# Optimization experiments

Hardware: AMD Instinct MI355X
Metric: run time of the kernel (lower is better)

Reference implementation:

```python
import jax, jax.numpy as jnp
import numpy as np

LATENT = 128
HEADS = 4
HEAD_DIM = LATENT // HEADS
NUM_BUCKETS = 32
MAX_DISTANCE = 100000
B, N = 8, 2048


def relative_position_bucket(qpos, kpos):
    """T5-style bidirectional relative position bucketing.
    qpos, kpos: [B, N] int -> buckets [B, N, N] int32 in [0, NUM_BUCKETS).
    """
    rel = kpos[:, None, :] - qpos[:, :, None]  # [B, Nq, Nk]
    half = NUM_BUCKETS // 2
    buckets = (rel > 0).astype(jnp.int32) * half
    arel = jnp.abs(rel)
    max_exact = half // 2
    is_small = arel < max_exact
    # log-spaced buckets for larger distances
    large = max_exact + (
        jnp.log(jnp.maximum(arel, 1).astype(jnp.float32) / max_exact)
        / np.log(MAX_DISTANCE / max_exact)
        * (half - max_exact)
    ).astype(jnp.int32)
    large = jnp.minimum(large, half - 1)
    return buckets + jnp.where(is_small, arel.astype(jnp.int32), large)


def setup_inputs() -> dict:
    key = jax.random.key(0)
    ks = jax.random.split(key, 12)
    s = 0.02
    x = jax.random.normal(ks[0], (B, N, LATENT), dtype=jnp.float32)
    positions = jnp.sort(jax.random.randint(ks[1], (B, N), 0, 1000000), axis=-1)
    mask = jnp.ones((B, N), dtype=bool)
    Wq = jax.random.normal(ks[2], (LATENT, LATENT), dtype=jnp.float32) * s
    bq = jax.random.normal(ks[3], (LATENT,), dtype=jnp.float32) * s
    Wk = jax.random.normal(ks[4], (LATENT, LATENT), dtype=jnp.float32) * s
    bk = jax.random.normal(ks[5], (LATENT,), dtype=jnp.float32) * s
    Wv = jax.random.normal(ks[6], (LATENT, LATENT), dtype=jnp.float32) * s
    bv = jax.random.normal(ks[7], (LATENT,), dtype=jnp.float32) * s
    pos_w = jax.random.normal(ks[8], (NUM_BUCKETS + 1, HEADS), dtype=jnp.float32) * s
    Wo = jax.random.normal(ks[9], (LATENT, LATENT), dtype=jnp.float32) * s
    bo = jax.random.normal(ks[10], (LATENT,), dtype=jnp.float32) * s
    return {"x": x, "positions": positions, "mask": mask,
            "Wq": Wq, "bq": bq, "Wk": Wk, "bk": bk, "Wv": Wv, "bv": bv,
            "pos_w": pos_w, "Wo": Wo, "bo": bo}


def reference(x, positions, mask, Wq, bq, Wk, bk, Wv, bv, pos_w, Wo, bo):
    b, n, _ = x.shape
    # QKV projections, split heads: [b, h, n, d]
    Q = (x @ Wq + bq).reshape(b, n, HEADS, HEAD_DIM).transpose(0, 2, 1, 3)
    K = (x @ Wk + bk).reshape(b, n, HEADS, HEAD_DIM).transpose(0, 2, 1, 3)
    V = (x @ Wv + bv).reshape(b, n, HEADS, HEAD_DIM).transpose(0, 2, 1, 3)
    scores = jnp.einsum("bhqd,bhkd->bhqk", Q, K) / jnp.sqrt(
        jnp.asarray(HEAD_DIM, dtype=x.dtype))
    buckets = relative_position_bucket(positions, positions)  # [b, n, n]
    bias = pos_w[buckets]                  # [b, n, n, h]
    scores = scores + bias.transpose(0, 3, 1, 2)  # [b, h, n, n]
    scores = jnp.where(mask[:, None, None, :], scores, -jnp.inf)
    attn = jax.nn.softmax(scores, axis=-1)
    attn = jnp.nan_to_num(attn, nan=0.0)
    attended = jnp.einsum("bhqk,bhkd->bhqd", attn, V)
    attended = attended.transpose(0, 2, 1, 3).reshape(b, n, LATENT)
    return attended @ Wo + bo
```

## Files before the change

### kernel.cpp

```cpp
#include <hip/hip_runtime.h>
#include <math.h>


#define LOG2E 1.4426950408889634f
#define QKV_SCALE 0.17677669529663687f
#define QS (QKV_SCALE * LOG2E)

typedef _Float16 half8 __attribute__((ext_vector_type(8)));
typedef float ffrag __attribute__((ext_vector_type(4)));

#if __has_builtin(__builtin_amdgcn_exp2f)
#define EXP2F __builtin_amdgcn_exp2f
#else
#define EXP2F exp2f
#endif

static __device__ __forceinline__ unsigned short f16bits(float f) {
    return __builtin_bit_cast(unsigned short, (_Float16)f);
}
static __device__ __forceinline__ float h16f(unsigned int bits) {
    return (float)__builtin_bit_cast(_Float16, (unsigned short)(bits & 0xFFFFu));
}
static __device__ __forceinline__ unsigned int pk2(float a, float b) {
    return __builtin_bit_cast(unsigned int, __builtin_amdgcn_cvt_pkrtz(a, b));
}
static __device__ __forceinline__ void async_cp16(const unsigned short* g, unsigned short* l) {
    __builtin_amdgcn_global_load_lds(
        (const __attribute__((address_space(1))) unsigned int*)g,
        (__attribute__((address_space(3))) unsigned int*)l, 16, 0, 0);
}

__device__ __constant__ int SN_TAB[32] = {
     -2000000000,
    -30755, -9458, -2908, -894, -275, -84, -26,
    -7, -6, -5, -4, -3, -2, -1,
    0,
    1, 2, 3, 4, 5, 6, 7,
    8,
    27, 85, 276, 895, 2909, 9459, 30756,
    2000000000 };

__global__ __launch_bounds__(256)
void prep_seg_kernel(const float* __restrict__ Wq, const float* __restrict__ Wk,
                     const float* __restrict__ Wv, const float* __restrict__ Wo,
                     const float* __restrict__ bq, const float* __restrict__ bk,
                     const float* __restrict__ bv,
                     const int* __restrict__ positions,
                     unsigned short* __restrict__ Wt_qkv,
                     unsigned short* __restrict__ Wt_o,
                     float* __restrict__ bias_qkv,
                     unsigned int* __restrict__ segtab)
{
    if (blockIdx.x < 256) {
        const int e = blockIdx.x * 256 + threadIdx.x;
        const int m = e >> 14, r = e & 16383;
        const int c = r >> 7, k = r & 127;
        float v;
        if (m == 0)      v = Wq[k * 128 + c] * QS;
        else if (m == 1) v = Wk[k * 128 + c];
        else if (m == 2) v = Wv[k * 128 + c];
        else             v = Wo[k * 128 + c];
        if (m < 3) Wt_qkv[(m * 128 + c) * 128 + k] = f16bits(v);
        else       Wt_o[c * 128 + k] = f16bits(v);
        if (e < 128)      bias_qkv[e] = bq[e] * QS;
        else if (e < 256) bias_qkv[e] = bk[e - 128];
        else if (e < 384) bias_qkv[e] = bv[e - 256];
        return;
    }
    const int gid = (blockIdx.x - 256) * 256 + threadIdx.x;
    const int row = gid >> 5;
    const int s = gid & 31;
    const int b = row >> 11;
    const int* kp = positions + b * 2048;
    const int qp = kp[row & 2047];
    const int bucket = (s < 15) ? (15 - s) : (s == 15 ? 0 : s + 1);
    if (s == 31) { segtab[row * 32 + s] = (2048u << 16) | 31u; return; }
    const int target = qp + SN_TAB[s + 1];
    int lo = 0, hi = 2048;
    while (lo < hi) { const int mid = (lo + hi) >> 1; if (kp[mid] < target) lo = mid + 1; else hi = mid; }
    segtab[row * 32 + s] = ((unsigned)lo << 16) | (unsigned)bucket;
}

__global__ __launch_bounds__(512)
void qkv_mfma(const float* __restrict__ x, const unsigned short* __restrict__ Wt,
              const float* __restrict__ bias_qkv,
              unsigned short* __restrict__ Qb, unsigned short* __restrict__ Kb,
              unsigned short* __restrict__ Vg2)
{
    __shared__ __align__(16) unsigned short Xs[64 * 136];
    const int tid = threadIdx.x;
    const int token0 = blockIdx.x * 64;
    #pragma unroll
    for (int it = 0; it < 4; ++it) {
        const int f = tid + it * 512;
        const int row = f >> 5, k0 = (f & 31) << 2;
        const float4 xv = *(const float4*)(x + (size_t)(token0 + row) * 128 + k0);
        uint2 u;
        u.x = pk2(xv.x, xv.y);
        u.y = pk2(xv.z, xv.w);
        *(uint2*)(Xs + row * 136 + k0) = u;
    }
    __syncthreads();

    const int wave = tid >> 6, lane = tid & 63;
    const int lq = lane & 15, quad = lane >> 4;
    const int b = token0 >> 11;
    const int n0 = token0 & 2047;

    #pragma unroll
    for (int j = 0; j < 3; ++j) {
        const int ct = wave + j * 8;
        const int colbase = ct * 16;
        half8 wf[4];
        #pragma unroll
        for (int ks = 0; ks < 4; ++ks)
            wf[ks] = *(const half8*)(Wt + (colbase + lq) * 128 + ks * 32 + quad * 8);

        if (ct < 16) {
            const int c0q = colbase + quad * 4;
            const float4 bv = *(const float4*)(bias_qkv + c0q);
            #pragma unroll
            for (int msub = 0; msub < 4; ++msub) {
                ffrag acc = {bv.x, bv.y, bv.z, bv.w};
                #pragma unroll
                for (int ks = 0; ks < 4; ++ks) {
                    const half8 xf = *(const half8*)(Xs + (msub * 16 + lq) * 136 + ks * 32 + quad * 8);
                    acc = __builtin_amdgcn_mfma_f32_16x16x32_f16(wf[ks], xf, acc, 0, 0, 0);
                }
                const int n = n0 + msub * 16 + lq;
                const int c0 = c0q & 127;
                const int h = c0 >> 5, d = c0 & 31;
                const ushort4 v4 = make_ushort4(f16bits(acc[0]), f16bits(acc[1]),
                                                f16bits(acc[2]), f16bits(acc[3]));
                unsigned short* base = (ct < 8) ? Qb : Kb;
                *(ushort4*)(base + ((size_t)(b * 4 + h) * 2048 + n) * 32 + d) = v4;
            }
        } else {
            const float bias = bias_qkv[colbase + lq];
            const int c2 = colbase + lq - 256;
            const int h = c2 >> 5, d = c2 & 31;
            const size_t bhh = (size_t)(b * 4 + h);
            #pragma unroll
            for (int msub = 0; msub < 4; ++msub) {
                ffrag acc = {bias, bias, bias, bias};
                #pragma unroll
                for (int ks = 0; ks < 4; ++ks) {
                    const half8 xf = *(const half8*)(Xs + (msub * 16 + lq) * 136 + ks * 32 + quad * 8);
                    acc = __builtin_amdgcn_mfma_f32_16x16x32_f16(xf, wf[ks], acc, 0, 0, 0);
                }
                const int n = n0 + msub * 16 + quad * 4;
                const int chunk = n >> 7, kloc = n & 127;
                const int win = kloc >> 5, rem = kloc & 31;
                const int half = rem >> 4, pg = (rem >> 2) & 3;
                const int G = d * 16 + ((win * 4 + pg) ^ (d & 15));
                const size_t off = ((bhh * 16 + chunk) * 512 + G) * 8 + half * 4;
                const ushort4 v4 = make_ushort4(f16bits(acc[0]), f16bits(acc[1]),
                                                f16bits(acc[2]), f16bits(acc[3]));
                *(ushort4*)(Vg2 + off) = v4;
            }
        }
    }
}

__global__ __launch_bounds__(512, 4)
void attn_kernel(const unsigned short* __restrict__ Qb,
                 const unsigned short* __restrict__ Kb,
                 const unsigned short* __restrict__ Vg2,
                 const unsigned int* __restrict__ segtab,
                 const float* __restrict__ pos_w,
                 unsigned short* __restrict__ att)
{
    __shared__ __align__(16) unsigned short VB[2][2][4096];
    __shared__ unsigned int Sg[128 * 32];

    const int tid = threadIdx.x;
    const int wave = __builtin_amdgcn_readfirstlane(tid >> 6);
    const int lane = tid & 63;
    const int lq = lane & 15, quad = lane >> 4;
    const int group = wave >> 2, wg = wave & 3;

    const int qt = blockIdx.x & 15;
    const int bh = blockIdx.x >> 4;
    const int b = bh >> 2, h = bh & 3;
    const int q0 = qt * 128;

    const unsigned short* Kg = Kb + (size_t)bh * 2048 * 32;
    const unsigned short* Vgb = Vg2 + (size_t)bh * 65536;

    #pragma unroll
    for (int it = 0; it < 2; ++it) {
        const int g = (wg * 2 + it) * 64 + lane;
        async_cp16(Vgb + (size_t)group * 4096 + g * 8, &VB[group][0][(wg * 2 + it) * 512]);
    }

    {
        const unsigned int* src = segtab + ((size_t)b * 2048 + q0) * 32;
        #pragma unroll
        for (int it = 0; it < 2; ++it) {
            const int e4 = tid + it * 512;
            uint4 u = *(const uint4*)(src + e4 * 4);
            unsigned int* c = &u.x;
            const int row = e4 >> 3, s0 = (e4 & 7) * 4;
            const int rx = row & 31;
            #pragma unroll
            for (int i = 0; i < 4; ++i) {
                const float wf = __expf(pos_w[(c[i] & 0xFFFFu) * 4 + h]);
                Sg[row * 32 + ((s0 + i) ^ rx)] = (c[i] & 0xFFFF0000u) | f16bits(wf);
            }
        }
    }

    const int qa = q0 + wg * 32 + lq;
    const int qbn = qa + 16;
    const half8 qfa = *(const half8*)(Qb + ((size_t)bh * 2048 + qa) * 32 + quad * 8);
    const half8 qfb = *(const half8*)(Qb + ((size_t)bh * 2048 + qbn) * 32 + quad * 8);

    half8 ones;
    #pragma unroll
    for (int i = 0; i < 8; ++i) ones[i] = (_Float16)1.0f;

    ffrag o0a = {0.f,0.f,0.f,0.f}, o1a = {0.f,0.f,0.f,0.f}, o2a = {0.f,0.f,0.f,0.f};
    ffrag o0b = {0.f,0.f,0.f,0.f}, o1b = {0.f,0.f,0.f,0.f}, o2b = {0.f,0.f,0.f,0.f};
    int cura = -1, enda = 0; float wfa = 0.f;
    int curb = -1, endb = 0; float wfb = 0.f;
    const int rowa = wg * 32 + lq, rowb = rowa + 16;
    const int sga = rowa * 32, xa = rowa & 31;
    const int sgb = rowb * 32, xb = rowb & 31;

    half8 kA[4], kB[4];
    {
        const int kc0 = group * 128;
        #pragma unroll
        for (int j = 0; j < 4; ++j)
            kA[j] = *(const half8*)(Kg + (size_t)(kc0 + j * 16 + lq) * 32 + quad * 8);
    }

    __syncthreads();

    auto half_chunk = [&](const half8* karr, const unsigned short* vb, int kc, int w0) {
        const int c0 = (w0 * 4 + quad) ^ lq;
        const int c1 = (w0 * 4 + 4 + quad) ^ lq;
        const half8 A00 = *(const half8*)(vb + (lq * 16 + c0) * 8);
        const half8 A10 = *(const half8*)(vb + ((16 + lq) * 16 + c0) * 8);
        const half8 A01 = *(const half8*)(vb + (lq * 16 + c1) * 8);
        const half8 A11 = *(const half8*)(vb + ((16 + lq) * 16 + c1) * 8);
        const int kmax = kc + w0 * 32 + 63;
        const bool cross = __any(kmax >= enda) || __any(kmax >= endb);
        #pragma unroll
        for (int dw = 0; dw < 2; ++dw) {
            const int w = w0 + dw;
            unsigned int pua[4], pub[4];
            #pragma unroll
            for (int T = 0; T < 2; ++T) {
                const half8 kf = karr[dw * 2 + T];
                ffrag sa = {0.f,0.f,0.f,0.f}, sb = {0.f,0.f,0.f,0.f};
                sa = __builtin_amdgcn_mfma_f32_16x16x32_f16(kf, qfa, sa, 0, 0, 0);
                sb = __builtin_amdgcn_mfma_f32_16x16x32_f16(kf, qfb, sb, 0, 0, 0);
                float pa[4], pb[4];
                if (__builtin_expect(cross, 0)) {
                    const int kidx = kc + (w * 2 + T) * 16 + quad * 4;
                    #pragma unroll
                    for (int r = 0; r < 4; ++r) {
                        while (kidx + r >= enda) {
                            const unsigned int u = Sg[sga + ((++cura) ^ xa)];
                            enda = (int)(u >> 16); wfa = h16f(u);
                        }
                        pa[r] = EXP2F(sa[r]) * wfa;
                    }
                    #pragma unroll
                    for (int r = 0; r < 4; ++r) {
                        while (kidx + r >= endb) {
                            const unsigned int u = Sg[sgb + ((++curb) ^ xb)];
                            endb = (int)(u >> 16); wfb = h16f(u);
                        }
                        pb[r] = EXP2F(sb[r]) * wfb;
                    }
                } else {
                    #pragma unroll
                    for (int r = 0; r < 4; ++r) pa[r] = EXP2F(sa[r]) * wfa;
                    #pragma unroll
                    for (int r = 0; r < 4; ++r) pb[r] = EXP2F(sb[r]) * wfb;
                }
                pua[T * 2 + 0] = pk2(pa[0], pa[1]);
                pua[T * 2 + 1] = pk2(pa[2], pa[3]);
                pub[T * 2 + 0] = pk2(pb[0], pb[1]);
                pub[T * 2 + 1] = pk2(pb[2], pb[3]);
            }
            const half8 A0 = dw ? A01 : A00;
            const half8 A1 = dw ? A11 : A10;
            const half8 Ba = __builtin_bit_cast(half8, make_int4(pua[0], pua[1], pua[2], pua[3]));
            const half8 Bb = __builtin_bit_cast(half8, make_int4(pub[0], pub[1], pub[2], pub[3]));
            __builtin_amdgcn_s_setprio(1);
            o0a = __builtin_amdgcn_mfma_f32_16x16x32_f16(A0, Ba, o0a, 0, 0, 0);
            o1a = __builtin_amdgcn_mfma_f32_16x16x32_f16(A1, Ba, o1a, 0, 0, 0);
            o2a = __builtin_amdgcn_mfma_f32_16x16x32_f16(ones, Ba, o2a, 0, 0, 0);
            o0b = __builtin_amdgcn_mfma_f32_16x16x32_f16(A0, Bb, o0b, 0, 0, 0);
            o1b = __builtin_amdgcn_mfma_f32_16x16x32_f16(A1, Bb, o1b, 0, 0, 0);
            o2b = __builtin_amdgcn_mfma_f32_16x16x32_f16(ones, Bb, o2b, 0, 0, 0);
            __builtin_amdgcn_s_setprio(0);
        }
    };

    for (int i = 0; i < 8; ++i) {
        const int kc = (2 * i + group) * 128;
        const unsigned short* vb = &VB[group][i & 1][0];
        if (i < 7) {
            #pragma unroll
            for (int it = 0; it < 2; ++it) {
                const int g = (wg * 2 + it) * 64 + lane;
                async_cp16(Vgb + (size_t)(2 * i + group + 2) * 4096 + g * 8,
                           &VB[group][(i + 1) & 1][(wg * 2 + it) * 512]);
            }
        }
        #pragma unroll
        for (int j = 0; j < 4; ++j)
            kB[j] = *(const half8*)(Kg + (size_t)(kc + (4 + j) * 16 + lq) * 32 + quad * 8);

        half_chunk(kA, vb, kc, 0);

        const int kcn = (i < 7) ? kc + 256 : kc;
        #pragma unroll
        for (int j = 0; j < 4; ++j)
            kA[j] = *(const half8*)(Kg + (size_t)(kcn + j * 16 + lq) * 32 + quad * 8);

        half_chunk(kB, vb, kc, 2);
        __syncthreads();
    }

    float lsa = o2a[0], lsb = o2b[0];
    float* scr = (float*)&VB[0][0][0];
    if (group == 1) {
        float* s = scr + (wg * 64 + lane) * 18;
        #pragma unroll
        for (int j = 0; j < 4; ++j) {
            s[j] = o0a[j]; s[4 + j] = o1a[j]; s[8 + j] = o0b[j]; s[12 + j] = o1b[j];
        }
        s[16] = lsa; s[17] = lsb;
    }
    __syncthreads();
    if (group == 0) {
        const float* s = scr + (wg * 64 + lane) * 18;
        #pragma unroll
        for (int j = 0; j < 4; ++j) {
            o0a[j] += s[j]; o1a[j] += s[4 + j]; o0b[j] += s[8 + j]; o1b[j] += s[12 + j];
        }
        lsa += s[16]; lsb += s[17];
        const float inva = 1.0f / lsa;
        const float invb = 1.0f / lsb;

        unsigned short* da = att + (size_t)(b * 2048 + qa) * 128 + h * 32 + quad * 4;
        uint2 r0, r1;
        r0.x = pk2(o0a[0] * inva, o0a[1] * inva);
        r0.y = pk2(o0a[2] * inva, o0a[3] * inva);
        r1.x = pk2(o1a[0] * inva, o1a[1] * inva);
        r1.y = pk2(o1a[2] * inva, o1a[3] * inva);
        *(uint2*)da = r0;
        *(uint2*)(da + 16) = r1;

        unsigned short* db = att + (size_t)(b * 2048 + qbn) * 128 + h * 32 + quad * 4;
        r0.x = pk2(o0b[0] * invb, o0b[1] * invb);
        r0.y = pk2(o0b[2] * invb, o0b[3] * invb);
        r1.x = pk2(o1b[0] * invb, o1b[1] * invb);
        r1.y = pk2(o1b[2] * invb, o1b[3] * invb);
        *(uint2*)db = r0;
        *(uint2*)(db + 16) = r1;
    }
}

__global__ __launch_bounds__(512)
void out_mfma(const unsigned short* __restrict__ att,
              const unsigned short* __restrict__ Wt_o,
              const float* __restrict__ bo, float* __restrict__ out)
{
    __shared__ __align__(16) unsigned short Xs[64 * 136];
    const int tid = threadIdx.x;
    const int token0 = blockIdx.x * 64;
    #pragma unroll
    for (int it = 0; it < 2; ++it) {
        const int f = tid + it * 512;
        const int row = f >> 4, k0 = (f & 15) << 3;
        const uint4 v = *(const uint4*)(att + (size_t)(token0 + row) * 128 + k0);
        *(uint4*)(Xs + row * 136 + k0) = v;
    }
    __syncthreads();

    const int wave = tid >> 6, lane = tid & 63;
    const int lq = lane & 15, quad = lane >> 4;
    const int colbase = wave * 16;

    half8 wf[4];
    #pragma unroll
    for (int ks = 0; ks < 4; ++ks)
        wf[ks] = *(const half8*)(Wt_o + (colbase + lq) * 128 + ks * 32 + quad * 8);
    const float4 bv = *(const float4*)(bo + colbase + quad * 4);

    #pragma unroll
    for (int msub = 0; msub < 4; ++msub) {
        ffrag acc = {bv.x, bv.y, bv.z, bv.w};
        #pragma unroll
        for (int ks = 0; ks < 4; ++ks) {
            const half8 xf = *(const half8*)(Xs + (msub * 16 + lq) * 136 + ks * 32 + quad * 8);
            acc = __builtin_amdgcn_mfma_f32_16x16x32_f16(wf[ks], xf, acc, 0, 0, 0);
        }
        const int c0 = colbase + quad * 4;
        *(float4*)(out + (size_t)(token0 + msub * 16 + lq) * 128 + c0) =
            make_float4(acc[0], acc[1], acc[2], acc[3]);
    }
}

extern "C" void kernel_launch(void* const* d_in, const int* in_sizes, int n_in,
                              void* d_out, int out_size, void* d_ws, size_t ws_size,
                              hipStream_t stream)
{
    const float* x         = (const float*)d_in[0];
    const int*   positions = (const int*)d_in[1];
    const float* Wq = (const float*)d_in[3];
    const float* bq = (const float*)d_in[4];
    const float* Wk = (const float*)d_in[5];
    const float* bk = (const float*)d_in[6];
    const float* Wv = (const float*)d_in[7];
    const float* bv = (const float*)d_in[8];
    const float* pw = (const float*)d_in[9];
    const float* Wo = (const float*)d_in[10];
    const float* bo = (const float*)d_in[11];
    float* out = (float*)d_out;

    unsigned short* Qb  = (unsigned short*)d_ws;
    unsigned short* Kb  = Qb + 2097152;
    unsigned short* Vg2 = Kb + 2097152;
    unsigned short* att = Vg2 + 2097152;
    unsigned int* segtab = (unsigned int*)(att + 2097152);
    unsigned short* Wt_qkv = (unsigned short*)(segtab + 524288);
    unsigned short* Wt_o = Wt_qkv + 49152;
    float* bias_qkv = (float*)(Wt_o + 16384);

    prep_seg_kernel<<<2304, 256, 0, stream>>>(Wq, Wk, Wv, Wo, bq, bk, bv, positions,
                                              Wt_qkv, Wt_o, bias_qkv, segtab);
    qkv_mfma<<<256, 512, 0, stream>>>(x, Wt_qkv, bias_qkv, Qb, Kb, Vg2);
    attn_kernel<<<512, 512, 0, stream>>>(Qb, Kb, Vg2, segtab, pw, att);
    out_mfma<<<256, 512, 0, stream>>>(att, Wt_o, bo, out);
}
```

Before: 150.7 us.

## Split attention over key halves and fold position bias into score accumulator

The attention kernel now splits each (batch, head, query-tile) over two key halves, doubling the grid to 1024 blocks. Each block writes unnormalized fp32 partial outputs and row sums, and the output projection kernel combines the two halves and normalizes before its GEMM. The bias is now kept in log2 domain and preloaded into the MFMA accumulator, so the exp already includes it and the per-element multiply is dropped. The cost is an extra fp32 partial buffer written and read through global memory, plus a fixed per-block prologue paid twice.

```diff
diff --git a/kernel.cpp b/kernel.cpp
--- a/kernel.cpp
+++ b/kernel.cpp
@@ -168,7 +168,7 @@
                  const unsigned short* __restrict__ Vg2,
                  const unsigned int* __restrict__ segtab,
                  const float* __restrict__ pos_w,
-                 unsigned short* __restrict__ att)
+                 float* __restrict__ P, float* __restrict__ D)
 {
     __shared__ __align__(16) unsigned short VB[2][2][4096];
     __shared__ unsigned int Sg[128 * 32];
@@ -180,9 +180,12 @@
     const int group = wave >> 2, wg = wave & 3;
 
     const int qt = blockIdx.x & 15;
-    const int bh = blockIdx.x >> 4;
+    const int kh = (blockIdx.x >> 4) & 1;
+    const int bh = blockIdx.x >> 5;
     const int b = bh >> 2, h = bh & 3;
     const int q0 = qt * 128;
+    const int k0 = kh * 1024;
+    const int ch0 = kh * 8;
 
     const unsigned short* Kg = Kb + (size_t)bh * 2048 * 32;
     const unsigned short* Vgb = Vg2 + (size_t)bh * 65536;
@@ -190,7 +193,7 @@
     #pragma unroll
     for (int it = 0; it < 2; ++it) {
         const int g = (wg * 2 + it) * 64 + lane;
-        async_cp16(Vgb + (size_t)group * 4096 + g * 8, &VB[group][0][(wg * 2 + it) * 512]);
+        async_cp16(Vgb + (size_t)(ch0 + group) * 4096 + g * 8, &VB[group][0][(wg * 2 + it) * 512]);
     }
 
     {
@@ -204,8 +207,8 @@
             const int rx = row & 31;
             #pragma unroll
             for (int i = 0; i < 4; ++i) {
-                const float wf = __expf(pos_w[(c[i] & 0xFFFFu) * 4 + h]);
-                Sg[row * 32 + ((s0 + i) ^ rx)] = (c[i] & 0xFFFF0000u) | f16bits(wf);
+                const float lw = pos_w[(c[i] & 0xFFFFu) * 4 + h] * LOG2E;
+                Sg[row * 32 + ((s0 + i) ^ rx)] = (c[i] & 0xFFFF0000u) | f16bits(lw);
             }
         }
     }
@@ -221,15 +224,16 @@
 
     ffrag o0a = {0.f,0.f,0.f,0.f}, o1a = {0.f,0.f,0.f,0.f}, o2a = {0.f,0.f,0.f,0.f};
     ffrag o0b = {0.f,0.f,0.f,0.f}, o1b = {0.f,0.f,0.f,0.f}, o2b = {0.f,0.f,0.f,0.f};
-    int cura = -1, enda = 0; float wfa = 0.f;
-    int curb = -1, endb = 0; float wfb = 0.f;
+    int cura = -1, enda = 0; float lwa = 0.f, lwa_base = 0.f;
+    int curb = -1, endb = 0; float lwb = 0.f, lwb_base = 0.f;
+    ffrag lwfa = {0.f,0.f,0.f,0.f}, lwfb = {0.f,0.f,0.f,0.f};
     const int rowa = wg * 32 + lq, rowb = rowa + 16;
     const int sga = rowa * 32, xa = rowa & 31;
     const int sgb = rowb * 32, xb = rowb & 31;
 
     half8 kA[4], kB[4];
     {
-        const int kc0 = group * 128;
+        const int kc0 = k0 + group * 128;
         #pragma unroll
         for (int j = 0; j < 4; ++j)
             kA[j] = *(const half8*)(Kg + (size_t)(kc0 + j * 16 + lq) * 32 + quad * 8);
@@ -253,9 +257,8 @@
             #pragma unroll
             for (int T = 0; T < 2; ++T) {
                 const half8 kf = karr[dw * 2 + T];
-                ffrag sa = {0.f,0.f,0.f,0.f}, sb = {0.f,0.f,0.f,0.f};
-                sa = __builtin_amdgcn_mfma_f32_16x16x32_f16(kf, qfa, sa, 0, 0, 0);
-                sb = __builtin_amdgcn_mfma_f32_16x16x32_f16(kf, qfb, sb, 0, 0, 0);
+                ffrag sa = __builtin_amdgcn_mfma_f32_16x16x32_f16(kf, qfa, lwfa, 0, 0, 0);
+                ffrag sb = __builtin_amdgcn_mfma_f32_16x16x32_f16(kf, qfb, lwfb, 0, 0, 0);
                 float pa[4], pb[4];
                 if (__builtin_expect(cross, 0)) {
                     const int kidx = kc + (w * 2 + T) * 16 + quad * 4;
@@ -263,23 +266,25 @@
                     for (int r = 0; r < 4; ++r) {
                         while (kidx + r >= enda) {
                             const unsigned int u = Sg[sga + ((++cura) ^ xa)];
-                            enda = (int)(u >> 16); wfa = h16f(u);
+                            enda = (int)(u >> 16); lwa = h16f(u);
                         }
-                        pa[r] = EXP2F(sa[r]) * wfa;
+                        pa[r] = EXP2F(sa[r] + (lwa - lwa_base));
                     }
                     #pragma unroll
                     for (int r = 0; r < 4; ++r) {
                         while (kidx + r >= endb) {
                             const unsigned int u = Sg[sgb + ((++curb) ^ xb)];
-                            endb = (int)(u >> 16); wfb = h16f(u);
+                            endb = (int)(u >> 16); lwb = h16f(u);
                         }
-                        pb[r] = EXP2F(sb[r]) * wfb;
+                        pb[r] = EXP2F(sb[r] + (lwb - lwb_base));
                     }
+                    if (lwa != lwa_base) { lwfa = (ffrag){lwa, lwa, lwa, lwa}; lwa_base = lwa; }
+                    if (lwb != lwb_base) { lwfb = (ffrag){lwb, lwb, lwb, lwb}; lwb_base = lwb; }
                 } else {
                     #pragma unroll
-                    for (int r = 0; r < 4; ++r) pa[r] = EXP2F(sa[r]) * wfa;
+                    for (int r = 0; r < 4; ++r) pa[r] = EXP2F(sa[r]);
                     #pragma unroll
-                    for (int r = 0; r < 4; ++r) pb[r] = EXP2F(sb[r]) * wfb;
+                    for (int r = 0; r < 4; ++r) pb[r] = EXP2F(sb[r]);
                 }
                 pua[T * 2 + 0] = pk2(pa[0], pa[1]);
                 pua[T * 2 + 1] = pk2(pa[2], pa[3]);
@@ -301,14 +306,14 @@
         }
     };
 
-    for (int i = 0; i < 8; ++i) {
-        const int kc = (2 * i + group) * 128;
+    for (int i = 0; i < 4; ++i) {
+        const int kc = k0 + (2 * i + group) * 128;
         const unsigned short* vb = &VB[group][i & 1][0];
-        if (i < 7) {
+        if (i < 3) {
             #pragma unroll
             for (int it = 0; it < 2; ++it) {
                 const int g = (wg * 2 + it) * 64 + lane;
-                async_cp16(Vgb + (size_t)(2 * i + group + 2) * 4096 + g * 8,
+                async_cp16(Vgb + (size_t)(ch0 + 2 * i + group + 2) * 4096 + g * 8,
                            &VB[group][(i + 1) & 1][(wg * 2 + it) * 512]);
             }
         }
@@ -318,7 +323,7 @@
 
         half_chunk(kA, vb, kc, 0);
 
-        const int kcn = (i < 7) ? kc + 256 : kc;
+        const int kcn = (i < 3) ? kc + 256 : kc;
         #pragma unroll
         for (int j = 0; j < 4; ++j)
             kA[j] = *(const half8*)(Kg + (size_t)(kcn + j * 16 + lq) * 32 + quad * 8);
@@ -345,30 +350,22 @@
             o0a[j] += s[j]; o1a[j] += s[4 + j]; o0b[j] += s[8 + j]; o1b[j] += s[12 + j];
         }
         lsa += s[16]; lsb += s[17];
-        const float inva = 1.0f / lsa;
-        const float invb = 1.0f / lsb;
-
-        unsigned short* da = att + (size_t)(b * 2048 + qa) * 128 + h * 32 + quad * 4;
-        uint2 r0, r1;
-        r0.x = pk2(o0a[0] * inva, o0a[1] * inva);
-        r0.y = pk2(o0a[2] * inva, o0a[3] * inva);
-        r1.x = pk2(o1a[0] * inva, o1a[1] * inva);
-        r1.y = pk2(o1a[2] * inva, o1a[3] * inva);
-        *(uint2*)da = r0;
-        *(uint2*)(da + 16) = r1;
-
-        unsigned short* db = att + (size_t)(b * 2048 + qbn) * 128 + h * 32 + quad * 4;
-        r0.x = pk2(o0b[0] * invb, o0b[1] * invb);
-        r0.y = pk2(o0b[2] * invb, o0b[3] * invb);
-        r1.x = pk2(o1b[0] * invb, o1b[1] * invb);
-        r1.y = pk2(o1b[2] * invb, o1b[3] * invb);
-        *(uint2*)db = r0;
-        *(uint2*)(db + 16) = r1;
+
+        const size_t pba = (((size_t)(b * 2048 + qa) * 4 + h) * 2 + kh) * 32;
+        *(ffrag*)(P + pba + quad * 4) = o0a;
+        *(ffrag*)(P + pba + 16 + quad * 4) = o1a;
+        const size_t pbb = (((size_t)(b * 2048 + qbn) * 4 + h) * 2 + kh) * 32;
+        *(ffrag*)(P + pbb + quad * 4) = o0b;
+        *(ffrag*)(P + pbb + 16 + quad * 4) = o1b;
+        if (quad == 0) {
+            D[((size_t)(b * 2048 + qa) * 4 + h) * 2 + kh] = lsa;
+            D[((size_t)(b * 2048 + qbn) * 4 + h) * 2 + kh] = lsb;
+        }
     }
 }
 
 __global__ __launch_bounds__(512)
-void out_mfma(const unsigned short* __restrict__ att,
+void out_mfma(const float* __restrict__ P, const float* __restrict__ D,
               const unsigned short* __restrict__ Wt_o,
               const float* __restrict__ bo, float* __restrict__ out)
 {
@@ -376,11 +373,21 @@
     const int tid = threadIdx.x;
     const int token0 = blockIdx.x * 64;
     #pragma unroll
-    for (int it = 0; it < 2; ++it) {
-        const int f = tid + it * 512;
-        const int row = f >> 4, k0 = (f & 15) << 3;
-        const uint4 v = *(const uint4*)(att + (size_t)(token0 + row) * 128 + k0);
-        *(uint4*)(Xs + row * 136 + k0) = v;
+    for (int it = 0; it < 4; ++it) {
+        const int u = tid + it * 512;
+        const int row = u >> 5;
+        const int c0 = (u & 31) * 4;
+        const int h = c0 >> 5, d0 = c0 & 31;
+        const size_t gq = (size_t)(token0 + row);
+        const float* pb = P + (gq * 4 + h) * 64;
+        const ffrag v0 = *(const ffrag*)(pb + d0);
+        const ffrag v1 = *(const ffrag*)(pb + 32 + d0);
+        const float2 dl = *(const float2*)(D + (gq * 4 + h) * 2);
+        const float inv = 1.0f / (dl.x + dl.y);
+        uint2 r;
+        r.x = pk2((v0[0] + v1[0]) * inv, (v0[1] + v1[1]) * inv);
+        r.y = pk2((v0[2] + v1[2]) * inv, (v0[3] + v1[3]) * inv);
+        *(uint2*)(Xs + row * 136 + c0) = r;
     }
     __syncthreads();
 
@@ -428,8 +435,9 @@
     unsigned short* Qb  = (unsigned short*)d_ws;
     unsigned short* Kb  = Qb + 2097152;
     unsigned short* Vg2 = Kb + 2097152;
-    unsigned short* att = Vg2 + 2097152;
-    unsigned int* segtab = (unsigned int*)(att + 2097152);
+    float* P = (float*)(Vg2 + 2097152);
+    float* D = P + 4194304;
+    unsigned int* segtab = (unsigned int*)(D + 131072);
     unsigned short* Wt_qkv = (unsigned short*)(segtab + 524288);
     unsigned short* Wt_o = Wt_qkv + 49152;
     float* bias_qkv = (float*)(Wt_o + 16384);
@@ -437,6 +445,6 @@
     prep_seg_kernel<<<2304, 256, 0, stream>>>(Wq, Wk, Wv, Wo, bq, bk, bv, positions,
                                               Wt_qkv, Wt_o, bias_qkv, segtab);
     qkv_mfma<<<256, 512, 0, stream>>>(x, Wt_qkv, bias_qkv, Qb, Kb, Vg2);
-    attn_kernel<<<512, 512, 0, stream>>>(Qb, Kb, Vg2, segtab, pw, att);
-    out_mfma<<<256, 512, 0, stream>>>(att, Wt_o, bo, out);
-}
+    attn_kernel<<<1024, 512, 0, stream>>>(Qb, Kb, Vg2, segtab, pw, P, D);
+    out_mfma<<<256, 512, 0, stream>>>(P, D, Wt_o, bo, out);
+}
```

Result: slower. 186.7 us (+23.8%).
